# Performance work log

Measured on AMD Instinct MI355X. Metric: run time of the kernel, lower is better.

Reference implementation:

```python
import jax, jax.numpy as jnp
import numpy as np
import math

B, S, D, H = 4, 1024, 512, 8
DK = D // H
NEG = -1e32


def setup_inputs() -> dict:
    key = jax.random.key(0)
    ks = jax.random.split(key, 16)
    f = lambda k, shape: jax.random.normal(k, shape, dtype=jnp.float32)
    w = 1.0 / math.sqrt(D)  # xavier-ish scale
    return {
        'query_mean': f(ks[0], (B, S, D)),
        'query_cov': f(ks[1], (B, S, D)),
        'key_mean': f(ks[2], (B, S, D)),
        'key_cov': f(ks[3], (B, S, D)),
        'values_mean': f(ks[4], (B, S, D)),
        'values_cov': f(ks[5], (B, S, D)),
        'Wk_mean': f(ks[6], (D, D)) * w, 'bk_mean': jnp.zeros((D,), jnp.float32),
        'Wk_cov': f(ks[7], (D, D)) * w, 'bk_cov': jnp.zeros((D,), jnp.float32),
        'Wv_mean': f(ks[8], (D, D)) * w, 'bv_mean': jnp.zeros((D,), jnp.float32),
        'Wv_cov': f(ks[9], (D, D)) * w, 'bv_cov': jnp.zeros((D,), jnp.float32),
        'Wo_mean': f(ks[10], (D, D)) * w, 'bo_mean': jnp.zeros((D,), jnp.float32),
        'Wo_cov': f(ks[11], (D, D)) * w, 'bo_cov': jnp.zeros((D,), jnp.float32),
        'gammas': f(ks[12], (H, 1, 1)) * 0.1,
        'mask': jnp.tril(jnp.ones((1, 1, S, S), dtype=jnp.int32)),
    }


def _forward(query_mean, query_cov, key_mean, key_cov, values_mean, values_cov,
             Wk_mean, bk_mean, Wk_cov, bk_cov, Wv_mean, bv_mean, Wv_cov, bv_cov,
             Wo_mean, bo_mean, Wo_cov, bo_cov, gammas, mask):
    def heads(x, W, b):  # [B,S,D] -> [B,H,S,DK]
        return (x @ W + b).reshape(B, S, H, DK).transpose(0, 2, 1, 3)

    # kq_same=True: queries and keys share the k linears
    qm = heads(query_mean, Wk_mean, bk_mean)
    qc = heads(query_cov, Wk_cov, bk_cov)
    km = heads(key_mean, Wk_mean, bk_mean)
    kc = heads(key_cov, Wk_cov, bk_cov)
    vm = heads(values_mean, Wv_mean, bv_mean)
    vc = heads(values_cov, Wv_cov, bv_cov)

    inv = 1.0 / math.sqrt(DK)
    sm = jnp.einsum('bhqd,bhkd->bhqk', qm, km) * inv  # [B,H,S,S]
    sc = jnp.einsum('bhqd,bhkd->bhqk', qc, kc) * inv

    maskf = mask.astype(jnp.float32)
    # position_effect[i,j] = |j - i|
    pos = jnp.abs(jnp.arange(S)[None, :] - jnp.arange(S)[:, None]).astype(jnp.float32)[None, None]

    def dist_scores(s):
        p = jax.nn.softmax(jnp.where(mask == 0, NEG, s), axis=-1) * maskf
        cum = jnp.cumsum(p, axis=-1)
        tot = jnp.sum(p, axis=-1, keepdims=True)
        return jnp.sqrt(jnp.clip((tot - cum) * pos, 0.0, None))

    dm = jax.lax.stop_gradient(dist_scores(sm))  # torch no_grad + detach
    dc = jax.lax.stop_gradient(dist_scores(sc))

    gv = -jax.nn.softplus(gammas)[None]  # [1,H,1,1]
    em = jnp.clip(jnp.exp(dm * gv), 1e-5, 1e5)
    ec = jnp.clip(jnp.exp(dc * gv), 1e-5, 1e5)

    am = jax.nn.softmax(jnp.where(mask == 0, NEG, sm * em), axis=-1)
    ac = jax.nn.softmax(jnp.where(mask == 0, NEG, sc * ec), axis=-1)

    om = jnp.einsum('bhqk,bhkd->bhqd', am, vm).transpose(0, 2, 1, 3).reshape(B, S, D)
    oc = jnp.einsum('bhqk,bhkd->bhqd', ac, vc).transpose(0, 2, 1, 3).reshape(B, S, D)
    return om @ Wo_mean + bo_mean, oc @ Wo_cov + bo_cov


def reference(query_mean, query_cov, key_mean, key_cov, values_mean, values_cov,
              Wk_mean, bk_mean, Wk_cov, bk_cov, Wv_mean, bv_mean, Wv_cov, bv_cov,
              Wo_mean, bo_mean, Wo_cov, bo_cov, gammas, mask):
    return _forward(query_mean, query_cov, key_mean, key_cov, values_mean, values_cov,
                    Wk_mean, bk_mean, Wk_cov, bk_cov, Wv_mean, bv_mean, Wv_cov, bv_cov,
                    Wo_mean, bo_mean, Wo_cov, bo_cov, gammas, mask)
```

## Files before the change

kernel.cpp:

```cpp
#include <hip/hip_runtime.h>
#include <hip/hip_bf16.h>
#include <math.h>

constexpr int B_  = 4;
constexpr int S_  = 1024;
constexpr int D_  = 512;
constexpr int H_  = 8;
constexpr int DK_ = 64;
constexpr int MROWS_ = B_ * S_;
constexpr size_t SZ_ = (size_t)B_ * H_ * S_ * DK_;
constexpr size_t WSZ_ = (size_t)D_ * D_;

typedef __attribute__((ext_vector_type(8))) short bf16x8;
typedef __attribute__((ext_vector_type(4))) float f32x4;

__device__ __forceinline__ float bf2f(unsigned short u) {
  union { unsigned int u; float f; } v; v.u = (unsigned int)u << 16; return v.f;
}
__device__ __forceinline__ unsigned short f2bf(float f) {
  union { float f; unsigned int u; } v; v.f = f;
  unsigned int r = v.u + 0x7FFFu + ((v.u >> 16) & 1u);
  return (unsigned short)(r >> 16);
}
__device__ __forceinline__ unsigned short f2bf_ru(float f) {
  union { float f; unsigned int u; } v; v.f = f;
  return (unsigned short)((v.u + 0x8000u) >> 16);
}

__device__ __forceinline__ float ex2(float x) {
#if __has_builtin(__builtin_amdgcn_exp2f)
  return __builtin_amdgcn_exp2f(x);
#else
  float r; asm("v_exp_f32 %0, %1" : "=v"(r) : "v"(x)); return r;
#endif
}
__device__ __forceinline__ float fsqrt_raw(float x) {
#if __has_builtin(__builtin_amdgcn_sqrtf)
  return __builtin_amdgcn_sqrtf(x);
#else
  float r; asm("v_sqrt_f32 %0, %1" : "=v"(r) : "v"(x)); return r;
#endif
}
__device__ __forceinline__ float frcp_raw(float x) {
#if __has_builtin(__builtin_amdgcn_rcpf)
  return __builtin_amdgcn_rcpf(x);
#else
  float r; asm("v_rcp_f32 %0, %1" : "=v"(r) : "v"(x)); return r;
#endif
}

template <int CTRL>
__device__ __forceinline__ float dpp_mov_f(float x) {
  return __builtin_bit_cast(float,
      __builtin_amdgcn_update_dpp(0, __builtin_bit_cast(int, x), CTRL, 0xF, 0xF, true));
}
__device__ __forceinline__ float scan16(float v) {
  v += dpp_mov_f<0x111>(v);
  v += dpp_mov_f<0x112>(v);
  v += dpp_mov_f<0x114>(v);
  v += dpp_mov_f<0x118>(v);
  return v;
}
__device__ __forceinline__ float red16(float v) {
  v += dpp_mov_f<0x128>(v);
  v += dpp_mov_f<0x124>(v);
  v += dpp_mov_f<0x122>(v);
  v += dpp_mov_f<0x121>(v);
  return v;
}
__device__ __forceinline__ float bcast15(float v) {
  return __builtin_bit_cast(float,
      __builtin_amdgcn_ds_swizzle(__builtin_bit_cast(int, v), 0x01F0));
}

struct TpArgs { const float* W[4]; unsigned short* out[4]; };

__global__ __launch_bounds__(256) void wtrans(TpArgs a) {
  const int z = blockIdx.z;
  const float* __restrict__ W = a.W[z];
  unsigned short* __restrict__ out = a.out[z];
  __shared__ float T[64][65];
  const int tid = threadIdx.x;
  const int tx = blockIdx.x & 7, ty = blockIdx.x >> 3;
  const int k0 = ty * 64, n0 = tx * 64;
#pragma unroll
  for (int i = 0; i < 4; ++i) {
    const int idx = tid + i * 256;
    const int r = idx >> 4, c4 = (idx & 15) * 4;
    const float4 w = *(const float4*)&W[(size_t)(k0 + r) * D_ + n0 + c4];
    T[r][c4 + 0] = w.x; T[r][c4 + 1] = w.y; T[r][c4 + 2] = w.z; T[r][c4 + 3] = w.w;
  }
  __syncthreads();
#pragma unroll
  for (int i = 0; i < 4; ++i) {
    const int idx = tid + i * 256;
    const int n = idx >> 4, kc = (idx & 15) * 4;
    ushort4 pk;
    pk.x = f2bf(T[kc + 0][n]); pk.y = f2bf(T[kc + 1][n]);
    pk.z = f2bf(T[kc + 2][n]); pk.w = f2bf(T[kc + 3][n]);
    *(ushort4*)&out[(size_t)(n0 + n) * D_ + k0 + kc] = pk;
  }
}

struct ProjArgs {
  const float* A[6]; const unsigned short* Wt[6]; const float* bias[6];
  unsigned short* out[6]; int vmode[6];
};

__global__ __launch_bounds__(256) void proj_mfma(ProjArgs args) {
  const int z = blockIdx.z;
  const float* __restrict__ A = args.A[z];
  const unsigned short* __restrict__ Wt = args.Wt[z];
  const float* __restrict__ bias = args.bias[z];
  unsigned short* __restrict__ out = args.out[z];
  const int vmode = args.vmode[z];

  __shared__ unsigned short Abuf[128][40];
  __shared__ unsigned short Bbuf[128][40];
  const int tid = threadIdx.x, wv = tid >> 6, lane = tid & 63;
  const int quad = lane >> 4, l16 = lane & 15;
  const int wm = wv >> 1, wn = wv & 1;
  const int n0 = blockIdx.x * 128, m0 = blockIdx.y * 128;

  f32x4 acc[4][4];
#pragma unroll
  for (int i = 0; i < 4; ++i)
#pragma unroll
    for (int j = 0; j < 4; ++j) acc[i][j] = (f32x4){0.f, 0.f, 0.f, 0.f};

  for (int kt = 0; kt < 16; ++kt) {
    const int k0 = kt * 32;
    __syncthreads();
#pragma unroll
    for (int i = 0; i < 4; ++i) {
      const int idx = tid + i * 256;
      const int m = idx >> 3, c = idx & 7;
      const float4 av = *(const float4*)&A[(size_t)(m0 + m) * D_ + k0 + c * 4];
      ushort4 p;
      p.x = f2bf(av.x); p.y = f2bf(av.y); p.z = f2bf(av.z); p.w = f2bf(av.w);
      *(ushort4*)&Abuf[m][c * 4] = p;
    }
#pragma unroll
    for (int i = 0; i < 2; ++i) {
      const int idx = tid + i * 256;
      const int n = idx >> 2, c = idx & 3;
      *(uint4*)&Bbuf[n][c * 8] = *(const uint4*)&Wt[(size_t)(n0 + n) * D_ + k0 + c * 8];
    }
    __syncthreads();

    bf16x8 af[4], bfr[4];
#pragma unroll
    for (int i = 0; i < 4; ++i) af[i] = *(const bf16x8*)&Abuf[wm * 64 + i * 16 + l16][quad * 8];
#pragma unroll
    for (int j = 0; j < 4; ++j) bfr[j] = *(const bf16x8*)&Bbuf[wn * 64 + j * 16 + l16][quad * 8];
#pragma unroll
    for (int i = 0; i < 4; ++i)
#pragma unroll
      for (int j = 0; j < 4; ++j)
        acc[i][j] = __builtin_amdgcn_mfma_f32_16x16x32_bf16(af[i], bfr[j], acc[i][j], 0, 0, 0);
  }

#pragma unroll
  for (int j = 0; j < 4; ++j) {
    const int col = n0 + wn * 64 + j * 16 + l16;
    const float bv = bias[col];
    const int h = col >> 6, dk = col & 63;
#pragma unroll
    for (int i = 0; i < 4; ++i) {
      const int mbase = m0 + wm * 64 + i * 16 + quad * 4;
      const int b = mbase >> 10;
      if (!vmode) {
#pragma unroll
        for (int r = 0; r < 4; ++r) {
          const int s = (mbase + r) & 1023;
          out[(((size_t)b * H_ + h) * S_ + s) * DK_ + dk] = f2bf(acc[i][j][r] + bv);
        }
      } else {
        const int s = mbase & 1023;
        ushort4 pk;
        pk.x = f2bf(acc[i][j][0] + bv); pk.y = f2bf(acc[i][j][1] + bv);
        pk.z = f2bf(acc[i][j][2] + bv); pk.w = f2bf(acc[i][j][3] + bv);
        *(ushort4*)&out[(((size_t)b * H_ + h) * DK_ + dk) * S_ + s] = pk;
      }
    }
  }
}

struct OutArgs {
  const unsigned short* A[2]; const unsigned short* Wt[2];
  const float* bias[2]; float* out[2];
};

__global__ __launch_bounds__(256) void out_mfma(OutArgs args) {
  const int z = blockIdx.z;
  const unsigned short* __restrict__ A = args.A[z];
  const unsigned short* __restrict__ Wt = args.Wt[z];
  const float* __restrict__ bias = args.bias[z];
  float* __restrict__ out = args.out[z];

  __shared__ unsigned short Abuf[128][40];
  __shared__ unsigned short Bbuf[128][40];
  const int tid = threadIdx.x, wv = tid >> 6, lane = tid & 63;
  const int quad = lane >> 4, l16 = lane & 15;
  const int wm = wv >> 1, wn = wv & 1;
  const int n0 = blockIdx.x * 128, m0 = blockIdx.y * 128;

  f32x4 acc[4][4];
#pragma unroll
  for (int i = 0; i < 4; ++i)
#pragma unroll
    for (int j = 0; j < 4; ++j) acc[i][j] = (f32x4){0.f, 0.f, 0.f, 0.f};

  for (int kt = 0; kt < 16; ++kt) {
    const int k0 = kt * 32;
    __syncthreads();
#pragma unroll
    for (int i = 0; i < 2; ++i) {
      const int idx = tid + i * 256;
      const int m = idx >> 2, c = idx & 3;
      *(uint4*)&Abuf[m][c * 8] = *(const uint4*)&A[(size_t)(m0 + m) * D_ + k0 + c * 8];
    }
#pragma unroll
    for (int i = 0; i < 2; ++i) {
      const int idx = tid + i * 256;
      const int n = idx >> 2, c = idx & 3;
      *(uint4*)&Bbuf[n][c * 8] = *(const uint4*)&Wt[(size_t)(n0 + n) * D_ + k0 + c * 8];
    }
    __syncthreads();

    bf16x8 af[4], bfr[4];
#pragma unroll
    for (int i = 0; i < 4; ++i) af[i] = *(const bf16x8*)&Abuf[wm * 64 + i * 16 + l16][quad * 8];
#pragma unroll
    for (int j = 0; j < 4; ++j) bfr[j] = *(const bf16x8*)&Bbuf[wn * 64 + j * 16 + l16][quad * 8];
#pragma unroll
    for (int i = 0; i < 4; ++i)
#pragma unroll
      for (int j = 0; j < 4; ++j)
        acc[i][j] = __builtin_amdgcn_mfma_f32_16x16x32_bf16(af[i], bfr[j], acc[i][j], 0, 0, 0);
  }

#pragma unroll
  for (int j = 0; j < 4; ++j) {
    const int col = n0 + wn * 64 + j * 16 + l16;
    const float bv = bias[col];
#pragma unroll
    for (int i = 0; i < 4; ++i) {
      const int mbase = m0 + wm * 64 + i * 16 + quad * 4;
#pragma unroll
      for (int r = 0; r < 4; ++r)
        out[(size_t)(mbase + r) * D_ + col] = acc[i][j][r] + bv;
    }
  }
}

__global__ __launch_bounds__(512) void attn_mfma(
    const unsigned short* __restrict__ qkv, const float* __restrict__ gammas,
    unsigned short* __restrict__ Obase)
{
  __shared__ unsigned short Ps[8][16][72];

  const int tid = threadIdx.x;
  const int w = tid >> 6, lane = tid & 63, quad = lane >> 4, l16 = lane & 15;
  const int bh = blockIdx.x;
  const int pair = blockIdx.y;
  const int ch = blockIdx.z;
  const int qt = (w < 4) ? (15 - pair) : pair;
  const int wq = w & 3;
  const int q0 = qt << 6;
  const int b = bh >> 3, h = bh & 7;

  constexpr float SC_ = 0.125f * 1.4426950408889634f;
  constexpr float LOG2E_ = 1.4426950408889634f;

  const unsigned short* Q  = qkv + (size_t)ch * 3 * SZ_ + (size_t)bh * S_ * DK_;
  const unsigned short* K  = qkv + (size_t)ch * 3 * SZ_ + SZ_ + (size_t)bh * S_ * DK_;
  const unsigned short* Vt = qkv + (size_t)ch * 3 * SZ_ + 2 * SZ_ + (size_t)bh * (size_t)DK_ * S_;
  unsigned short* O = Obase + (size_t)ch * SZ_;

  const float g = gammas[h];
  const float gv2 = -(fmaxf(g, 0.f) + log1pf(__expf(-fabsf(g)))) * LOG2E_;

  const unsigned short* Qrow = Q + (size_t)(q0 + wq * 16 + l16) * DK_;
  const bf16x8 qf0 = *(const bf16x8*)(Qrow + quad * 8);
  const bf16x8 qf1 = *(const bf16x8*)(Qrow + 32 + quad * 8);
  const int myrow = q0 + wq * 16 + quad * 4;

  float Tacc[4] = {0.f, 0.f, 0.f, 0.f};
  for (int kt = 0; kt <= qt; ++kt) {
    f32x4 sa[4];
#pragma unroll
    for (int cb = 0; cb < 4; ++cb) {
      const unsigned short* Kr = K + (size_t)(kt * 64 + cb * 16 + l16) * DK_;
      const bf16x8 kf0 = *(const bf16x8*)(Kr + quad * 8);
      const bf16x8 kf1 = *(const bf16x8*)(Kr + 32 + quad * 8);
      f32x4 a = {0.f, 0.f, 0.f, 0.f};
      a = __builtin_amdgcn_mfma_f32_16x16x32_bf16(qf0, kf0, a, 0, 0, 0);
      a = __builtin_amdgcn_mfma_f32_16x16x32_bf16(qf1, kf1, a, 0, 0, 0);
      sa[cb] = a;
    }
    if (kt == qt) {
#pragma unroll
      for (int cb = 0; cb < 4; ++cb)
#pragma unroll
        for (int r = 0; r < 4; ++r) {
          float e = ex2(sa[cb][r] * SC_);
          if ((kt * 64 + cb * 16 + l16) > (myrow + r)) e = 0.f;
          Tacc[r] += e;
        }
    } else {
#pragma unroll
      for (int cb = 0; cb < 4; ++cb)
#pragma unroll
        for (int r = 0; r < 4; ++r)
          Tacc[r] += ex2(sa[cb][r] * SC_);
    }
  }
  float invT[4];
#pragma unroll
  for (int r = 0; r < 4; ++r) invT[r] = frcp_raw(red16(Tacc[r]));

  float carry[4] = {0.f, 0.f, 0.f, 0.f};
  float l2a[4] = {0.f, 0.f, 0.f, 0.f};
  f32x4 oacc[4];
#pragma unroll
  for (int cb = 0; cb < 4; ++cb) oacc[cb] = (f32x4){0.f, 0.f, 0.f, 0.f};

  for (int kt = 0; kt <= qt; ++kt) {
    bf16x8 vf0[4], vf1[4];
#pragma unroll
    for (int cb = 0; cb < 4; ++cb) {
      const unsigned short* Vr = Vt + (size_t)(cb * 16 + l16) * S_ + kt * 64;
      vf0[cb] = *(const bf16x8*)(Vr + quad * 8);
      vf1[cb] = *(const bf16x8*)(Vr + 32 + quad * 8);
    }

    f32x4 sa[4];
#pragma unroll
    for (int cb = 0; cb < 4; ++cb) {
      const unsigned short* Kr = K + (size_t)(kt * 64 + cb * 16 + l16) * DK_;
      const bf16x8 kf0 = *(const bf16x8*)(Kr + quad * 8);
      const bf16x8 kf1 = *(const bf16x8*)(Kr + 32 + quad * 8);
      f32x4 a = {0.f, 0.f, 0.f, 0.f};
      a = __builtin_amdgcn_mfma_f32_16x16x32_bf16(qf0, kf0, a, 0, 0, 0);
      a = __builtin_amdgcn_mfma_f32_16x16x32_bf16(qf1, kf1, a, 0, 0, 0);
      sa[cb] = a;
    }
#pragma unroll
    for (int cb = 0; cb < 4; ++cb)
#pragma unroll
      for (int r = 0; r < 4; ++r) sa[cb][r] *= SC_;
    if (kt == qt) {
#pragma unroll
      for (int cb = 0; cb < 4; ++cb)
#pragma unroll
        for (int r = 0; r < 4; ++r)
          if ((kt * 64 + cb * 16 + l16) > (myrow + r)) sa[cb][r] = -1e30f;
    }

#pragma unroll
    for (int r = 0; r < 4; ++r) {
      float v0 = scan16(ex2(sa[0][r]));
      float v1 = scan16(ex2(sa[1][r]));
      float v2 = scan16(ex2(sa[2][r]));
      float v3 = scan16(ex2(sa[3][r]));
      const float tt0 = bcast15(v0), tt1 = bcast15(v1);
      const float tt2 = bcast15(v2), tt3 = bcast15(v3);
      const float base = carry[r];
      const float p01 = tt0 + tt1, p012 = p01 + tt2;
      const float cum0 = (base + v0) * invT[r];
      const float cum1 = (base + tt0 + v1) * invT[r];
      const float cum2 = (base + p01 + v2) * invT[r];
      const float cum3 = (base + p012 + v3) * invT[r];
      carry[r] = base + p012 + tt3;

      const float bpos = (float)(myrow + r) - (float)(kt * 64 + l16);
      float dd, st0, st1, st2, st3;
      dd = fsqrt_raw(fmaxf((1.f - cum0) * bpos, 0.f));
      st0 = sa[0][r] * fmaxf(ex2(dd * gv2), 1e-5f);
      dd = fsqrt_raw(fmaxf((1.f - cum1) * (bpos - 16.f), 0.f));
      st1 = sa[1][r] * fmaxf(ex2(dd * gv2), 1e-5f);
      dd = fsqrt_raw(fmaxf((1.f - cum2) * (bpos - 32.f), 0.f));
      st2 = sa[2][r] * fmaxf(ex2(dd * gv2), 1e-5f);
      dd = fsqrt_raw(fmaxf((1.f - cum3) * (bpos - 48.f), 0.f));
      st3 = sa[3][r] * fmaxf(ex2(dd * gv2), 1e-5f);

      const float w0 = ex2(st0), w1 = ex2(st1);
      const float w2 = ex2(st2), w3 = ex2(st3);
      l2a[r] += (w0 + w1) + (w2 + w3);
      const int prow = quad * 4 + r;
      Ps[w][prow][ 0 + l16] = f2bf_ru(w0);
      Ps[w][prow][16 + l16] = f2bf_ru(w1);
      Ps[w][prow][32 + l16] = f2bf_ru(w2);
      Ps[w][prow][48 + l16] = f2bf_ru(w3);
    }
    asm volatile("s_waitcnt lgkmcnt(0)" ::: "memory");

    const bf16x8 pf0 = *(const bf16x8*)&Ps[w][l16][quad * 8];
    const bf16x8 pf1 = *(const bf16x8*)&Ps[w][l16][32 + quad * 8];
#pragma unroll
    for (int cb = 0; cb < 4; ++cb) {
      oacc[cb] = __builtin_amdgcn_mfma_f32_16x16x32_bf16(pf0, vf0[cb], oacc[cb], 0, 0, 0);
      oacc[cb] = __builtin_amdgcn_mfma_f32_16x16x32_bf16(pf1, vf1[cb], oacc[cb], 0, 0, 0);
    }
  }

#pragma unroll
  for (int r = 0; r < 4; ++r) {
    const float inv = frcp_raw(red16(l2a[r]));
    const int srow = myrow + r;
    const size_t base = ((size_t)b * S_ + srow) * D_ + h * DK_;
    O[base +  0 + l16] = f2bf(oacc[0][r] * inv);
    O[base + 16 + l16] = f2bf(oacc[1][r] * inv);
    O[base + 32 + l16] = f2bf(oacc[2][r] * inv);
    O[base + 48 + l16] = f2bf(oacc[3][r] * inv);
  }
}

extern "C" void kernel_launch(void* const* d_in, const int* in_sizes, int n_in,
                              void* d_out, int out_size, void* d_ws, size_t ws_size,
                              hipStream_t stream) {
  const float* query_mean  = (const float*)d_in[0];
  const float* query_cov   = (const float*)d_in[1];
  const float* key_mean    = (const float*)d_in[2];
  const float* key_cov     = (const float*)d_in[3];
  const float* values_mean = (const float*)d_in[4];
  const float* values_cov  = (const float*)d_in[5];
  const float* Wk_mean = (const float*)d_in[6];
  const float* bk_mean = (const float*)d_in[7];
  const float* Wk_cov  = (const float*)d_in[8];
  const float* bk_cov  = (const float*)d_in[9];
  const float* Wv_mean = (const float*)d_in[10];
  const float* bv_mean = (const float*)d_in[11];
  const float* Wv_cov  = (const float*)d_in[12];
  const float* bv_cov  = (const float*)d_in[13];
  const float* Wo_mean = (const float*)d_in[14];
  const float* bo_mean = (const float*)d_in[15];
  const float* Wo_cov  = (const float*)d_in[16];
  const float* bo_cov  = (const float*)d_in[17];
  const float* gammas  = (const float*)d_in[18];

  unsigned short* qkv  = (unsigned short*)d_ws;
  unsigned short* obuf = qkv + 6 * SZ_;
  unsigned short* Wt4  = (unsigned short*)d_out;
  unsigned short* Wot  = qkv + 2 * SZ_;
  float* out = (float*)d_out;

  TpArgs t1;
  t1.W[0] = Wk_mean; t1.W[1] = Wv_mean; t1.W[2] = Wk_cov; t1.W[3] = Wv_cov;
  for (int i = 0; i < 4; ++i) t1.out[i] = Wt4 + (size_t)i * WSZ_;
  wtrans<<<dim3(64, 1, 4), 256, 0, stream>>>(t1);

  ProjArgs pa;
  const float* pA[6] = {query_mean, key_mean, values_mean, query_cov, key_cov, values_cov};
  const int   wIdx[6] = {0, 0, 1, 2, 2, 3};
  const float* pb[6] = {bk_mean, bk_mean, bv_mean, bk_cov, bk_cov, bv_cov};
  const int pv[6] = {0, 0, 1, 0, 0, 1};
  for (int i = 0; i < 6; ++i) {
    pa.A[i] = pA[i]; pa.Wt[i] = Wt4 + (size_t)wIdx[i] * WSZ_; pa.bias[i] = pb[i];
    pa.out[i] = qkv + (size_t)i * SZ_; pa.vmode[i] = pv[i];
  }
  proj_mfma<<<dim3(4, 32, 6), 256, 0, stream>>>(pa);

  attn_mfma<<<dim3(32, 8, 2), 512, 0, stream>>>(qkv, gammas, obuf);

  TpArgs t2;
  t2.W[0] = Wo_mean; t2.W[1] = Wo_cov; t2.W[2] = Wo_mean; t2.W[3] = Wo_cov;
  t2.out[0] = Wot; t2.out[1] = Wot + WSZ_; t2.out[2] = Wot; t2.out[3] = Wot + WSZ_;
  wtrans<<<dim3(64, 1, 2), 256, 0, stream>>>(t2);

  OutArgs oa;
  oa.A[0] = obuf;        oa.A[1] = obuf + SZ_;
  oa.Wt[0] = Wot;        oa.Wt[1] = Wot + WSZ_;
  oa.bias[0] = bo_mean;  oa.bias[1] = bo_cov;
  oa.out[0] = out;       oa.out[1] = out + (size_t)MROWS_ * D_;
  out_mfma<<<dim3(4, 32, 2), 256, 0, stream>>>(oa);
}
```

Baseline: 267.6 us.

## Software-pipeline PV MFMA one tile behind score computation with double-buffered P

```diff
diff --git a/kernel.cpp b/kernel.cpp
--- a/kernel.cpp
+++ b/kernel.cpp
@@ -258,7 +258,7 @@
     const unsigned short* __restrict__ qkv, const float* __restrict__ gammas,
     unsigned short* __restrict__ Obase)
 {
-  __shared__ unsigned short Ps[8][16][72];
+  __shared__ unsigned short Ps[8][2][16][72];
 
   const int tid = threadIdx.x;
   const int w = tid >> 6, lane = tid & 63, quad = lane >> 4, l16 = lane & 15;
@@ -328,11 +328,17 @@
 
   for (int kt = 0; kt <= qt; ++kt) {
     bf16x8 vf0[4], vf1[4];
-#pragma unroll
-    for (int cb = 0; cb < 4; ++cb) {
-      const unsigned short* Vr = Vt + (size_t)(cb * 16 + l16) * S_ + kt * 64;
-      vf0[cb] = *(const bf16x8*)(Vr + quad * 8);
-      vf1[cb] = *(const bf16x8*)(Vr + 32 + quad * 8);
+    bf16x8 pf0 = {}, pf1 = {};
+    if (kt > 0) {
+      const int tp = kt - 1;
+#pragma unroll
+      for (int cb = 0; cb < 4; ++cb) {
+        const unsigned short* Vr = Vt + (size_t)(cb * 16 + l16) * S_ + tp * 64;
+        vf0[cb] = *(const bf16x8*)(Vr + quad * 8);
+        vf1[cb] = *(const bf16x8*)(Vr + 32 + quad * 8);
+      }
+      pf0 = *(const bf16x8*)&Ps[w][tp & 1][l16][quad * 8];
+      pf1 = *(const bf16x8*)&Ps[w][tp & 1][l16][32 + quad * 8];
     }
 
     f32x4 sa[4];
@@ -389,15 +395,32 @@
       const float w2 = ex2(st2), w3 = ex2(st3);
       l2a[r] += (w0 + w1) + (w2 + w3);
       const int prow = quad * 4 + r;
-      Ps[w][prow][ 0 + l16] = f2bf_ru(w0);
-      Ps[w][prow][16 + l16] = f2bf_ru(w1);
-      Ps[w][prow][32 + l16] = f2bf_ru(w2);
-      Ps[w][prow][48 + l16] = f2bf_ru(w3);
-    }
-    asm volatile("s_waitcnt lgkmcnt(0)" ::: "memory");
-
-    const bf16x8 pf0 = *(const bf16x8*)&Ps[w][l16][quad * 8];
-    const bf16x8 pf1 = *(const bf16x8*)&Ps[w][l16][32 + quad * 8];
+      Ps[w][kt & 1][prow][ 0 + l16] = f2bf_ru(w0);
+      Ps[w][kt & 1][prow][16 + l16] = f2bf_ru(w1);
+      Ps[w][kt & 1][prow][32 + l16] = f2bf_ru(w2);
+      Ps[w][kt & 1][prow][48 + l16] = f2bf_ru(w3);
+    }
+
+    if (kt > 0) {
+#pragma unroll
+      for (int cb = 0; cb < 4; ++cb) {
+        oacc[cb] = __builtin_amdgcn_mfma_f32_16x16x32_bf16(pf0, vf0[cb], oacc[cb], 0, 0, 0);
+        oacc[cb] = __builtin_amdgcn_mfma_f32_16x16x32_bf16(pf1, vf1[cb], oacc[cb], 0, 0, 0);
+      }
+    }
+  }
+
+  {
+    const int tp = qt;
+    bf16x8 vf0[4], vf1[4];
+#pragma unroll
+    for (int cb = 0; cb < 4; ++cb) {
+      const unsigned short* Vr = Vt + (size_t)(cb * 16 + l16) * S_ + tp * 64;
+      vf0[cb] = *(const bf16x8*)(Vr + quad * 8);
+      vf1[cb] = *(const bf16x8*)(Vr + 32 + quad * 8);
+    }
+    const bf16x8 pf0 = *(const bf16x8*)&Ps[w][tp & 1][l16][quad * 8];
+    const bf16x8 pf1 = *(const bf16x8*)&Ps[w][tp & 1][l16][32 + quad * 8];
 #pragma unroll
     for (int cb = 0; cb < 4; ++cb) {
       oacc[cb] = __builtin_amdgcn_mfma_f32_16x16x32_bf16(pf0, vf0[cb], oacc[cb], 0, 0, 0);
```

Measured after the change: 271.5 us. About the same (+1.5%).
